# Optimization experiments

Measured on AMD Instinct MI355X. Metric: run time of the kernel, lower is better.

## Reference

```python
import math
import jax, jax.numpy as jnp
import numpy as np

N, C, H, Wsp = 128, 512, 28, 28
NCLS = 1000

def setup_inputs() -> dict:
    key = jax.random.key(0)
    k1, k2, k3 = jax.random.split(key, 3)
    feat = jax.random.normal(k1, (N, C, H, Wsp), dtype=jnp.float32)
    y = jax.random.randint(k2, (N,), 0, NCLS, dtype=jnp.int64)
    w = jax.random.normal(k3, (NCLS, C), dtype=jnp.float32) * 0.02  # Linear weight
    b = jnp.zeros((NCLS,), dtype=jnp.float32)                        # Linear bias
    return {"feat": feat, "y": y, "w": w, "b": b}

def reference(feat, y, w, b):
    # Probe(feat): global avg pool -> flatten -> linear
    pooled = feat.mean(axis=(2, 3))            # (N, C)
    pred_cas = pooled @ w.T + b                # (N, NCLS)
    # _get_mask_with_graph (training branch, y given).
    # logits(scores) = (scores * pooled_detached) @ w.T + b, so
    # d sum_n logits[n, y_n] / d scores[n, c] = w[y_n, c] * pooled[n, c] (closed form of autograd.grad).
    pooled_sg = jax.lax.stop_gradient(pooled)  # feat.detach() in original
    g = w[y] * pooled_sg                       # (N, C) grad wrt scores
    norm = jnp.linalg.norm(g, axis=1, keepdims=True)  # (N, 1)
    c = feat.shape[1]
    mask = 1.0 + g / norm * (math.sqrt(c) / 2.0)      # scores(=1) + normalized grad
    mask = jax.nn.softmax(mask, axis=1)        # (N, C)
    masked_feat = feat * mask[:, :, None, None]
    return masked_feat, pred_cas
```

## Files before the change

kernel.cpp:

```cpp
#include <hip/hip_runtime.h>
#include <math.h>

#define NB   128
#define CCH  512
#define HW   784
#define NCLS 1000
#define TOT4 12845056

__global__ __launch_bounds__(256) void k_pool(const float* __restrict__ feat,
                                              float* __restrict__ pooled) {
    int wv = threadIdx.x >> 6, lane = threadIdx.x & 63;
    int ch = blockIdx.x * 4 + wv;
    const float* src = feat + (size_t)ch * HW;
    float s = 0.f;
#pragma unroll
    for (int it = 0; it < 3; ++it) {
        float4 v = *reinterpret_cast<const float4*>(src + it * 256 + lane * 4);
        s += v.x + v.y + v.z + v.w;
    }
    if (lane < 4) {
        float4 v = *reinterpret_cast<const float4*>(src + 768 + lane * 4);
        s += v.x + v.y + v.z + v.w;
    }
#pragma unroll
    for (int o = 32; o; o >>= 1) s += __shfl_down(s, o, 64);
    if (lane == 0) pooled[ch] = s * (1.0f / 784.0f);
}

__global__ __launch_bounds__(256) void k_linear(const float* __restrict__ pooled,
                                                const float* __restrict__ w,
                                                const float* __restrict__ b,
                                                float* __restrict__ out) {
    int wv = threadIdx.x >> 6, lane = threadIdx.x & 63;
    int idx = blockIdx.x * 4 + wv;
    int n = idx / NCLS, cls = idx - n * NCLS;
    const float* wr = w + (size_t)cls * CCH;
    const float* pr = pooled + (size_t)n * CCH;
    float4 a0 = *reinterpret_cast<const float4*>(wr + lane * 8);
    float4 a1 = *reinterpret_cast<const float4*>(wr + lane * 8 + 4);
    float4 p0 = *reinterpret_cast<const float4*>(pr + lane * 8);
    float4 p1 = *reinterpret_cast<const float4*>(pr + lane * 8 + 4);
    float s = a0.x * p0.x + a0.y * p0.y + a0.z * p0.z + a0.w * p0.w
            + a1.x * p1.x + a1.y * p1.y + a1.z * p1.z + a1.w * p1.w;
#pragma unroll
    for (int o = 32; o; o >>= 1) s += __shfl_down(s, o, 64);
    if (lane == 0) out[idx] = s + b[cls];
}

__global__ __launch_bounds__(512) void k_mask(const float* __restrict__ pooled,
                                              const float* __restrict__ w,
                                              const int* __restrict__ y,
                                              float* __restrict__ mask) {
    __shared__ float red[8];
    __shared__ float bc;
    int n = blockIdx.x;
    int c = threadIdx.x;
    int lane = c & 63, wv = c >> 6;
    int cls = y[n];
    float g = w[(size_t)cls * CCH + c] * pooled[(size_t)n * CCH + c];

    float ss = g * g;
#pragma unroll
    for (int o = 32; o; o >>= 1) ss += __shfl_down(ss, o, 64);
    if (lane == 0) red[wv] = ss;
    __syncthreads();
    if (c == 0) { float t = 0.f; for (int i = 0; i < 8; ++i) t += red[i]; bc = sqrtf(t); }
    __syncthreads();
    float vv = 1.0f + g * (11.313708498984761f / bc);
    __syncthreads();

    float mx = vv;
#pragma unroll
    for (int o = 32; o; o >>= 1) mx = fmaxf(mx, __shfl_down(mx, o, 64));
    if (lane == 0) red[wv] = mx;
    __syncthreads();
    if (c == 0) { float t = red[0]; for (int i = 1; i < 8; ++i) t = fmaxf(t, red[i]); bc = t; }
    __syncthreads();
    float e = expf(vv - bc);
    __syncthreads();

    float se = e;
#pragma unroll
    for (int o = 32; o; o >>= 1) se += __shfl_down(se, o, 64);
    if (lane == 0) red[wv] = se;
    __syncthreads();
    if (c == 0) { float t = 0.f; for (int i = 0; i < 8; ++i) t += red[i]; bc = t; }
    __syncthreads();
    mask[(size_t)n * CCH + c] = e / bc;
}

__global__ __launch_bounds__(256) void k_apply(const float* __restrict__ feat,
                                               const float* __restrict__ mask,
                                               float* __restrict__ out) {
    unsigned int i = blockIdx.x * 256u + threadIdx.x;
    unsigned int ch = i / 196u;
    float m = mask[ch];
    float4 v = reinterpret_cast<const float4*>(feat)[i];
    v.x *= m; v.y *= m; v.z *= m; v.w *= m;
    reinterpret_cast<float4*>(out)[i] = v;
}

extern "C" void kernel_launch(void* const* d_in, const int* in_sizes, int n_in,
                              void* d_out, int out_size, void* d_ws, size_t ws_size,
                              hipStream_t stream) {
    const float* feat = (const float*)d_in[0];
    const int*   y    = (const int*)d_in[1];
    const float* w    = (const float*)d_in[2];
    const float* b    = (const float*)d_in[3];

    float* out_feat = (float*)d_out;
    float* out_pred = out_feat + (size_t)NB * CCH * HW;

    float* pooled = (float*)d_ws;
    float* maskp  = pooled + NB * CCH;

    k_pool  <<<(NB * CCH) / 4, 256, 0, stream>>>(feat, pooled);
    k_linear<<<(NB * NCLS) / 4, 256, 0, stream>>>(pooled, w, b, out_pred);
    k_mask  <<<NB, 512, 0, stream>>>(pooled, w, y, maskp);
    k_apply <<<TOT4 / 256, 256, 0, stream>>>(feat, maskp, out_feat);
}
```

Baseline: 128.6 us.

## Fuse linear and mask kernels, reuse pooled rows from LDS, nontemporal stores

Merges the linear-head and mask-softmax kernels into one launch. Blocks below LIN_BLOCKS compute the linear layer, and the remaining blocks compute the per-sample softmax mask. In the linear part, each block stages 8 pooled rows in shared memory so each weight row is reused across 8 samples instead of being reloaded once per (n, class) pair. The apply kernel now uses nontemporal stores for the large masked output to reduce cache pollution. The aim is to cut one launch and redundant weight traffic. The gain is small relative to the dominant memory-bound apply pass.

```diff
diff --git a/kernel.cpp b/kernel.cpp
--- a/kernel.cpp
+++ b/kernel.cpp
@@ -7,6 +7,8 @@
 #define NCLS 1000
 #define TOT4 12845056
 
+typedef float f32x4 __attribute__((ext_vector_type(4)));
+
 __global__ __launch_bounds__(256) void k_pool(const float* __restrict__ feat,
                                               float* __restrict__ pooled) {
     int wv = threadIdx.x >> 6, lane = threadIdx.x & 63;
@@ -15,11 +17,11 @@
     float s = 0.f;
 #pragma unroll
     for (int it = 0; it < 3; ++it) {
-        float4 v = *reinterpret_cast<const float4*>(src + it * 256 + lane * 4);
+        f32x4 v = *reinterpret_cast<const f32x4*>(src + it * 256 + lane * 4);
         s += v.x + v.y + v.z + v.w;
     }
     if (lane < 4) {
-        float4 v = *reinterpret_cast<const float4*>(src + 768 + lane * 4);
+        f32x4 v = *reinterpret_cast<const f32x4*>(src + 768 + lane * 4);
         s += v.x + v.y + v.z + v.w;
     }
 #pragma unroll
@@ -27,66 +29,87 @@
     if (lane == 0) pooled[ch] = s * (1.0f / 784.0f);
 }
 
-__global__ __launch_bounds__(256) void k_linear(const float* __restrict__ pooled,
-                                                const float* __restrict__ w,
-                                                const float* __restrict__ b,
-                                                float* __restrict__ out) {
-    int wv = threadIdx.x >> 6, lane = threadIdx.x & 63;
-    int idx = blockIdx.x * 4 + wv;
-    int n = idx / NCLS, cls = idx - n * NCLS;
-    const float* wr = w + (size_t)cls * CCH;
-    const float* pr = pooled + (size_t)n * CCH;
-    float4 a0 = *reinterpret_cast<const float4*>(wr + lane * 8);
-    float4 a1 = *reinterpret_cast<const float4*>(wr + lane * 8 + 4);
-    float4 p0 = *reinterpret_cast<const float4*>(pr + lane * 8);
-    float4 p1 = *reinterpret_cast<const float4*>(pr + lane * 8 + 4);
-    float s = a0.x * p0.x + a0.y * p0.y + a0.z * p0.z + a0.w * p0.w
-            + a1.x * p1.x + a1.y * p1.y + a1.z * p1.z + a1.w * p1.w;
+#define LIN_BLOCKS 4000
+__global__ __launch_bounds__(256) void k_head(const float* __restrict__ pooled,
+                                              const float* __restrict__ w,
+                                              const float* __restrict__ b,
+                                              const int* __restrict__ y,
+                                              float* __restrict__ pred,
+                                              float* __restrict__ mask) {
+    __shared__ float sp[4096];
+    int t = threadIdx.x, lane = t & 63, wv = t >> 6;
+
+    if (blockIdx.x < LIN_BLOCKS) {
+        int cb = blockIdx.x % 250;
+        int nb = blockIdx.x / 250;
+        const float* pbase = pooled + (size_t)nb * 8 * CCH;
 #pragma unroll
-    for (int o = 32; o; o >>= 1) s += __shfl_down(s, o, 64);
-    if (lane == 0) out[idx] = s + b[cls];
-}
+        for (int k = 0; k < 4; ++k)
+            *reinterpret_cast<f32x4*>(sp + k * 1024 + t * 4) =
+                *reinterpret_cast<const f32x4*>(pbase + k * 1024 + t * 4);
+        __syncthreads();
 
-__global__ __launch_bounds__(512) void k_mask(const float* __restrict__ pooled,
-                                              const float* __restrict__ w,
-                                              const int* __restrict__ y,
-                                              float* __restrict__ mask) {
-    __shared__ float red[8];
-    __shared__ float bc;
-    int n = blockIdx.x;
-    int c = threadIdx.x;
-    int lane = c & 63, wv = c >> 6;
-    int cls = y[n];
-    float g = w[(size_t)cls * CCH + c] * pooled[(size_t)n * CCH + c];
+        int cls = cb * 4 + wv;
+        const float* wr = w + (size_t)cls * CCH;
+        f32x4 a0 = *reinterpret_cast<const f32x4*>(wr + lane * 8);
+        f32x4 a1 = *reinterpret_cast<const f32x4*>(wr + lane * 8 + 4);
+        float bias = b[cls];
+        float s[8];
+#pragma unroll
+        for (int nn = 0; nn < 8; ++nn) {
+            f32x4 p0 = *reinterpret_cast<const f32x4*>(sp + nn * CCH + lane * 8);
+            f32x4 p1 = *reinterpret_cast<const f32x4*>(sp + nn * CCH + lane * 8 + 4);
+            s[nn] = a0.x * p0.x + a0.y * p0.y + a0.z * p0.z + a0.w * p0.w
+                  + a1.x * p1.x + a1.y * p1.y + a1.z * p1.z + a1.w * p1.w;
+        }
+#pragma unroll
+        for (int nn = 0; nn < 8; ++nn) {
+            float v = s[nn];
+#pragma unroll
+            for (int o = 32; o; o >>= 1) v += __shfl_down(v, o, 64);
+            if (lane == 0) pred[(size_t)(nb * 8 + nn) * NCLS + cls] = v + bias;
+        }
+    } else {
+        int n = blockIdx.x - LIN_BLOCKS;
+        int cls = y[n];
+        const float* wr = w + (size_t)cls * CCH;
+        const float* pr = pooled + (size_t)n * CCH;
+        float g0 = wr[t] * pr[t];
+        float g1 = wr[t + 256] * pr[t + 256];
 
-    float ss = g * g;
+        float ss = g0 * g0 + g1 * g1;
 #pragma unroll
-    for (int o = 32; o; o >>= 1) ss += __shfl_down(ss, o, 64);
-    if (lane == 0) red[wv] = ss;
-    __syncthreads();
-    if (c == 0) { float t = 0.f; for (int i = 0; i < 8; ++i) t += red[i]; bc = sqrtf(t); }
-    __syncthreads();
-    float vv = 1.0f + g * (11.313708498984761f / bc);
-    __syncthreads();
+        for (int o = 32; o; o >>= 1) ss += __shfl_down(ss, o, 64);
+        if (lane == 0) sp[wv] = ss;
+        __syncthreads();
+        if (t == 0) sp[8] = sqrtf(sp[0] + sp[1] + sp[2] + sp[3]);
+        __syncthreads();
+        float inv = 11.313708498984761f / sp[8];
+        float v0 = 1.0f + g0 * inv, v1 = 1.0f + g1 * inv;
+        __syncthreads();
 
-    float mx = vv;
+        float mx = fmaxf(v0, v1);
 #pragma unroll
-    for (int o = 32; o; o >>= 1) mx = fmaxf(mx, __shfl_down(mx, o, 64));
-    if (lane == 0) red[wv] = mx;
-    __syncthreads();
-    if (c == 0) { float t = red[0]; for (int i = 1; i < 8; ++i) t = fmaxf(t, red[i]); bc = t; }
-    __syncthreads();
-    float e = expf(vv - bc);
-    __syncthreads();
+        for (int o = 32; o; o >>= 1) mx = fmaxf(mx, __shfl_down(mx, o, 64));
+        if (lane == 0) sp[wv] = mx;
+        __syncthreads();
+        if (t == 0) sp[8] = fmaxf(fmaxf(sp[0], sp[1]), fmaxf(sp[2], sp[3]));
+        __syncthreads();
+        float m = sp[8];
+        float e0 = expf(v0 - m), e1 = expf(v1 - m);
+        __syncthreads();
 
-    float se = e;
+        float se = e0 + e1;
 #pragma unroll
-    for (int o = 32; o; o >>= 1) se += __shfl_down(se, o, 64);
-    if (lane == 0) red[wv] = se;
-    __syncthreads();
-    if (c == 0) { float t = 0.f; for (int i = 0; i < 8; ++i) t += red[i]; bc = t; }
-    __syncthreads();
-    mask[(size_t)n * CCH + c] = e / bc;
+        for (int o = 32; o; o >>= 1) se += __shfl_down(se, o, 64);
+        if (lane == 0) sp[wv] = se;
+        __syncthreads();
+        if (t == 0) sp[8] = sp[0] + sp[1] + sp[2] + sp[3];
+        __syncthreads();
+        float is = 1.0f / sp[8];
+        mask[(size_t)n * CCH + t] = e0 * is;
+        mask[(size_t)n * CCH + t + 256] = e1 * is;
+    }
 }
 
 __global__ __launch_bounds__(256) void k_apply(const float* __restrict__ feat,
@@ -95,9 +118,9 @@
     unsigned int i = blockIdx.x * 256u + threadIdx.x;
     unsigned int ch = i / 196u;
     float m = mask[ch];
-    float4 v = reinterpret_cast<const float4*>(feat)[i];
+    f32x4 v = reinterpret_cast<const f32x4*>(feat)[i];
     v.x *= m; v.y *= m; v.z *= m; v.w *= m;
-    reinterpret_cast<float4*>(out)[i] = v;
+    __builtin_nontemporal_store(v, reinterpret_cast<f32x4*>(out) + i);
 }
 
 extern "C" void kernel_launch(void* const* d_in, const int* in_sizes, int n_in,
@@ -114,8 +137,7 @@
     float* pooled = (float*)d_ws;
     float* maskp  = pooled + NB * CCH;
 
-    k_pool  <<<(NB * CCH) / 4, 256, 0, stream>>>(feat, pooled);
-    k_linear<<<(NB * NCLS) / 4, 256, 0, stream>>>(pooled, w, b, out_pred);
-    k_mask  <<<NB, 512, 0, stream>>>(pooled, w, y, maskp);
-    k_apply <<<TOT4 / 256, 256, 0, stream>>>(feat, maskp, out_feat);
+    k_pool <<<(NB * CCH) / 4, 256, 0, stream>>>(feat, pooled);
+    k_head <<<LIN_BLOCKS + NB, 256, 0, stream>>>(pooled, w, b, y, out_pred, maskp);
+    k_apply<<<TOT4 / 256, 256, 0, stream>>>(feat, maskp, out_feat);
 }
```

Result: faster. 106.1 us (-17.5%).

## Fuse pool, mask, linear and apply into one persistent kernel with grid barriers

Applied to the files above, without the earlier changes.

Replaces four kernels with a single persistent 256-block kernel. Each block holds a 64-channel slice of one image in registers, pools it, waits on a global atomic barrier, computes the softmax mask, and writes the scaled features from registers. This removes the second read of feat and the extra launches. The linear layer is spread across rounds, and a memset plus a spin barrier are added. The cost is a large register footprint (49 float4 per thread), possible spills, and reliance on all 256 blocks being co-resident.

```diff
diff --git a/kernel.cpp b/kernel.cpp
--- a/kernel.cpp
+++ b/kernel.cpp
@@ -5,99 +5,141 @@
 #define CCH  512
 #define HW   784
 #define NCLS 1000
-#define TOT4 12845056
+#define GRID 256
+#define RNDS 4
+#define IMGR 32
+#define K49  49
 
-__global__ __launch_bounds__(256) void k_pool(const float* __restrict__ feat,
-                                              float* __restrict__ pooled) {
-    int wv = threadIdx.x >> 6, lane = threadIdx.x & 63;
-    int ch = blockIdx.x * 4 + wv;
-    const float* src = feat + (size_t)ch * HW;
-    float s = 0.f;
-#pragma unroll
-    for (int it = 0; it < 3; ++it) {
-        float4 v = *reinterpret_cast<const float4*>(src + it * 256 + lane * 4);
-        s += v.x + v.y + v.z + v.w;
+typedef float f32x4 __attribute__((ext_vector_type(4)));
+
+__device__ __forceinline__ void grid_barrier(unsigned* bar, unsigned target) {
+    __syncthreads();
+    if (threadIdx.x == 0) {
+        __threadfence();
+        __hip_atomic_fetch_add(bar, 1u, __ATOMIC_ACQ_REL, __HIP_MEMORY_SCOPE_AGENT);
+        while (__hip_atomic_load(bar, __ATOMIC_ACQUIRE, __HIP_MEMORY_SCOPE_AGENT) < target)
+            __builtin_amdgcn_s_sleep(2);
     }
-    if (lane < 4) {
-        float4 v = *reinterpret_cast<const float4*>(src + 768 + lane * 4);
-        s += v.x + v.y + v.z + v.w;
-    }
-#pragma unroll
-    for (int o = 32; o; o >>= 1) s += __shfl_down(s, o, 64);
-    if (lane == 0) pooled[ch] = s * (1.0f / 784.0f);
+    __syncthreads();
 }
 
-__global__ __launch_bounds__(256) void k_linear(const float* __restrict__ pooled,
+__global__ __launch_bounds__(256, 2) void k_all(const float* __restrict__ feat,
+                                                const int* __restrict__ y,
                                                 const float* __restrict__ w,
-                                                const float* __restrict__ b,
-                                                float* __restrict__ out) {
-    int wv = threadIdx.x >> 6, lane = threadIdx.x & 63;
-    int idx = blockIdx.x * 4 + wv;
-    int n = idx / NCLS, cls = idx - n * NCLS;
-    const float* wr = w + (size_t)cls * CCH;
-    const float* pr = pooled + (size_t)n * CCH;
-    float4 a0 = *reinterpret_cast<const float4*>(wr + lane * 8);
-    float4 a1 = *reinterpret_cast<const float4*>(wr + lane * 8 + 4);
-    float4 p0 = *reinterpret_cast<const float4*>(pr + lane * 8);
-    float4 p1 = *reinterpret_cast<const float4*>(pr + lane * 8 + 4);
-    float s = a0.x * p0.x + a0.y * p0.y + a0.z * p0.z + a0.w * p0.w
-            + a1.x * p1.x + a1.y * p1.y + a1.z * p1.z + a1.w * p1.w;
+                                                const float* __restrict__ bias,
+                                                float* __restrict__ out,
+                                                float* __restrict__ pred,
+                                                float* __restrict__ pooled,
+                                                unsigned* __restrict__ bar) {
+    __shared__ float lds[12544];
+    float* red   = lds;
+    float* smask = lds + 6144;
+
+    const int t = threadIdx.x;
+    const int lane = t & 63, wv = t >> 6;
+    const int b = blockIdx.x;
+    const int nl = b >> 3;
+    const int q  = b & 7;
+
+    for (int r = 0; r < RNDS; ++r) {
+        const int n = r * IMGR + nl;
+        const size_t sbase = ((size_t)n * CCH + (q << 6)) * HW;
+        const f32x4* src4 = reinterpret_cast<const f32x4*>(feat + sbase);
+
+        f32x4 rdat[K49];
 #pragma unroll
-    for (int o = 32; o; o >>= 1) s += __shfl_down(s, o, 64);
-    if (lane == 0) out[idx] = s + b[cls];
-}
+        for (int k = 0; k < K49; ++k) rdat[k] = src4[k * 256 + t];
+#pragma unroll
+        for (int k = 0; k < K49; ++k) {
+            int i = k * 256 + t;
+            lds[i] = rdat[k].x + rdat[k].y + rdat[k].z + rdat[k].w;
+        }
+        __syncthreads();
+        {
+            float s = 0.f;
+            int base = (t >> 2) * 196 + (t & 3) * 49;
+#pragma unroll
+            for (int j = 0; j < K49; ++j) s += lds[base + j];
+            s += __shfl_xor(s, 1, 64);
+            s += __shfl_xor(s, 2, 64);
+            if ((t & 3) == 0)
+                pooled[(size_t)n * CCH + (q << 6) + (t >> 2)] = s * (1.0f / 784.0f);
+        }
+        grid_barrier(bar, (unsigned)(r + 1) * GRID);
 
-__global__ __launch_bounds__(512) void k_mask(const float* __restrict__ pooled,
-                                              const float* __restrict__ w,
-                                              const int* __restrict__ y,
-                                              float* __restrict__ mask) {
-    __shared__ float red[8];
-    __shared__ float bc;
-    int n = blockIdx.x;
-    int c = threadIdx.x;
-    int lane = c & 63, wv = c >> 6;
-    int cls = y[n];
-    float g = w[(size_t)cls * CCH + c] * pooled[(size_t)n * CCH + c];
+        {
+            int cls = y[n];
+            float p0 = pooled[(size_t)n * CCH + t];
+            float p1 = pooled[(size_t)n * CCH + t + 256];
+            float g0 = w[(size_t)cls * CCH + t] * p0;
+            float g1 = w[(size_t)cls * CCH + t + 256] * p1;
 
-    float ss = g * g;
+            float ss = g0 * g0 + g1 * g1;
 #pragma unroll
-    for (int o = 32; o; o >>= 1) ss += __shfl_down(ss, o, 64);
-    if (lane == 0) red[wv] = ss;
-    __syncthreads();
-    if (c == 0) { float t = 0.f; for (int i = 0; i < 8; ++i) t += red[i]; bc = sqrtf(t); }
-    __syncthreads();
-    float vv = 1.0f + g * (11.313708498984761f / bc);
-    __syncthreads();
+            for (int o = 32; o; o >>= 1) ss += __shfl_down(ss, o, 64);
+            if (lane == 0) red[wv] = ss;
+            __syncthreads();
+            if (t == 0) red[4] = sqrtf(red[0] + red[1] + red[2] + red[3]);
+            __syncthreads();
+            float inv = 11.313708498984761f / red[4];
+            float v0 = 1.0f + g0 * inv, v1 = 1.0f + g1 * inv;
+            __syncthreads();
 
-    float mx = vv;
+            float mx = fmaxf(v0, v1);
 #pragma unroll
-    for (int o = 32; o; o >>= 1) mx = fmaxf(mx, __shfl_down(mx, o, 64));
-    if (lane == 0) red[wv] = mx;
-    __syncthreads();
-    if (c == 0) { float t = red[0]; for (int i = 1; i < 8; ++i) t = fmaxf(t, red[i]); bc = t; }
-    __syncthreads();
-    float e = expf(vv - bc);
-    __syncthreads();
+            for (int o = 32; o; o >>= 1) mx = fmaxf(mx, __shfl_down(mx, o, 64));
+            if (lane == 0) red[wv] = mx;
+            __syncthreads();
+            if (t == 0) red[4] = fmaxf(fmaxf(red[0], red[1]), fmaxf(red[2], red[3]));
+            __syncthreads();
+            float mmax = red[4];
+            float e0 = expf(v0 - mmax), e1 = expf(v1 - mmax);
+            __syncthreads();
 
-    float se = e;
+            float se = e0 + e1;
 #pragma unroll
-    for (int o = 32; o; o >>= 1) se += __shfl_down(se, o, 64);
-    if (lane == 0) red[wv] = se;
-    __syncthreads();
-    if (c == 0) { float t = 0.f; for (int i = 0; i < 8; ++i) t += red[i]; bc = t; }
-    __syncthreads();
-    mask[(size_t)n * CCH + c] = e / bc;
-}
+            for (int o = 32; o; o >>= 1) se += __shfl_down(se, o, 64);
+            if (lane == 0) red[wv] = se;
+            __syncthreads();
+            if (t == 0) red[4] = red[0] + red[1] + red[2] + red[3];
+            __syncthreads();
+            float is = 1.0f / red[4];
+            smask[t] = e0 * is;
+            smask[t + 256] = e1 * is;
+            __syncthreads();
+        }
 
-__global__ __launch_bounds__(256) void k_apply(const float* __restrict__ feat,
-                                               const float* __restrict__ mask,
-                                               float* __restrict__ out) {
-    unsigned int i = blockIdx.x * 256u + threadIdx.x;
-    unsigned int ch = i / 196u;
-    float m = mask[ch];
-    float4 v = reinterpret_cast<const float4*>(feat)[i];
-    v.x *= m; v.y *= m; v.z *= m; v.w *= m;
-    reinterpret_cast<float4*>(out)[i] = v;
+        {
+            f32x4* dst4 = reinterpret_cast<f32x4*>(out + sbase);
+            const float* sm = smask + (q << 6);
+#pragma unroll
+            for (int k = 0; k < K49; ++k) {
+                unsigned int i = k * 256u + t;
+                float m = sm[i / 196u];
+                f32x4 v = rdat[k];
+                v.x *= m; v.y *= m; v.z *= m; v.w *= m;
+                __builtin_nontemporal_store(v, dst4 + i);
+            }
+        }
+
+        if (b < 250) {
+            int cls = b * 4 + wv;
+            const f32x4* wr4 = reinterpret_cast<const f32x4*>(w + (size_t)cls * CCH);
+            f32x4 a0 = wr4[lane * 2], a1 = wr4[lane * 2 + 1];
+            float bv = bias[cls];
+            for (int nn = 0; nn < IMGR; ++nn) {
+                int ni = r * IMGR + nn;
+                const f32x4* pr4 = reinterpret_cast<const f32x4*>(pooled + (size_t)ni * CCH);
+                f32x4 pp0 = pr4[lane * 2], pp1 = pr4[lane * 2 + 1];
+                float s = a0.x * pp0.x + a0.y * pp0.y + a0.z * pp0.z + a0.w * pp0.w
+                        + a1.x * pp1.x + a1.y * pp1.y + a1.z * pp1.z + a1.w * pp1.w;
+#pragma unroll
+                for (int o = 32; o; o >>= 1) s += __shfl_down(s, o, 64);
+                if (lane == 0) pred[(size_t)ni * NCLS + cls] = s + bv;
+            }
+        }
+        __syncthreads();
+    }
 }
 
 extern "C" void kernel_launch(void* const* d_in, const int* in_sizes, int n_in,
@@ -112,10 +154,8 @@
     float* out_pred = out_feat + (size_t)NB * CCH * HW;
 
     float* pooled = (float*)d_ws;
-    float* maskp  = pooled + NB * CCH;
+    unsigned* bar = (unsigned*)((char*)d_ws + 65536 * sizeof(float));
 
-    k_pool  <<<(NB * CCH) / 4, 256, 0, stream>>>(feat, pooled);
-    k_linear<<<(NB * NCLS) / 4, 256, 0, stream>>>(pooled, w, b, out_pred);
-    k_mask  <<<NB, 512, 0, stream>>>(pooled, w, y, maskp);
-    k_apply <<<TOT4 / 256, 256, 0, stream>>>(feat, maskp, out_feat);
+    hipMemsetAsync(bar, 0, 64, stream);
+    k_all<<<GRID, 256, 0, stream>>>(feat, y, w, b, out_feat, out_pred, pooled, bar);
 }
```

Result: slower. 243.7 us (+89.5%).
